# Optimization experiments

Hardware: AMD Instinct MI355X
Metric: run time of the kernel (lower is better)

Reference implementation:

```python
import jax, jax.numpy as jnp
import numpy as np

D = 1024
HEADS = 16
LN_EPS = 1e-5   # torch LayerNorm default
SHEP_EPS = 1e-4 # eps in shepards_MHA
SHEP_P = 2


def setup_inputs() -> dict:
    key = jax.random.key(0)
    k1, k2, k3 = jax.random.split(key, 3)
    b, t, d = 2, 2048, D
    X = jax.random.normal(k1, (b, t, d), dtype=jnp.float32)
    # Linear weights, scaled like torch default init (~U(-1/sqrt(fan_in), ...)) magnitude
    W_in = jax.random.normal(k2, (4 * d, d), dtype=jnp.float32) * (1.0 / np.sqrt(d))
    b_in = jnp.zeros((4 * d,), dtype=jnp.float32)
    W_out = jax.random.normal(k3, (d, d), dtype=jnp.float32) * (1.0 / np.sqrt(d))
    b_out = jnp.zeros((d,), dtype=jnp.float32)
    return {"X": X, "W_in": W_in, "b_in": b_in, "W_out": W_out, "b_out": b_out}


def _shepards_mha(Q, K, V):
    # Q,K,V: [b,h,t,dh]. Euclidean cdist via ||q||^2 + ||k||^2 - 2 q.k
    q2 = jnp.sum(Q * Q, axis=-1, keepdims=True)          # [b,h,t,1]
    k2 = jnp.sum(K * K, axis=-1, keepdims=True)          # [b,h,t,1]
    sq = q2 + jnp.swapaxes(k2, -1, -2) - 2.0 * jnp.einsum('bhqd,bhkd->bhqk', Q, K)
    dist = jnp.sqrt(jnp.maximum(sq, 0.0))                # [b,h,t,t]
    W = (SHEP_EPS + dist) ** (-SHEP_P)
    W = W / (SHEP_EPS + jnp.sum(W, axis=-1, keepdims=True))
    return jnp.einsum('bhqk,bhkd->bhqd', W, V)


def reference(X, W_in, b_in, W_out, b_out):
    b, t, d = X.shape
    h = HEADS
    dh = d // h
    # LayerNorm (no affine)
    mu = jnp.mean(X, axis=-1, keepdims=True)
    var = jnp.mean((X - mu) ** 2, axis=-1, keepdims=True)
    Xn = (X - mu) / jnp.sqrt(var + LN_EPS)
    # project_in: [b,t,4d]
    P = jnp.einsum('btd,ed->bte', Xn, W_in) + b_in
    # [b,t,h,4*dh] -> [b,h,t,4*dh]
    P = P.reshape(b, t, h, 4 * dh).transpose(0, 2, 1, 3)
    Q, K, V, G = jnp.split(P, 4, axis=-1)                # each [b,h,t,dh]
    A = _shepards_mha(Q, K, V)
    O = (G * A).transpose(0, 2, 1, 3).reshape(b, t, d)
    return X + jnp.einsum('btd,ed->bte', O, W_out) + b_out
```

## Files before the change

kernel.cpp:

```cpp
#include <hip/hip_runtime.h>

#define SEQ 2048
#define D_MODEL 1024
#define NTOK 4096
#define PROW 4096
#define DH 64
#define LN_EPS 1e-5f
#define SHEP_EPS 1e-4f

typedef __attribute__((ext_vector_type(8))) short bf16x8;
typedef __attribute__((ext_vector_type(4))) short s16x4;
typedef __attribute__((ext_vector_type(4))) float f32x4;

__device__ __forceinline__ unsigned short f2bf(float f) {
  union { float f; unsigned u; } v; v.f = f;
  unsigned r = v.u + 0x7fffu + ((v.u >> 16) & 1u);
  return (unsigned short)(r >> 16);
}
__device__ __forceinline__ float bf2f(unsigned short s) {
  union { unsigned u; float f; } v; v.u = ((unsigned)s) << 16;
  return v.f;
}
__device__ __forceinline__ void gload16(const void* g, void* l) {
  __builtin_amdgcn_global_load_lds(
      (const __attribute__((address_space(1))) unsigned int*)g,
      (__attribute__((address_space(3))) unsigned int*)l, 16, 0, 0);
}
__device__ __forceinline__ void gload4(const void* g, void* l) {
  __builtin_amdgcn_global_load_lds(
      (const __attribute__((address_space(1))) unsigned int*)g,
      (__attribute__((address_space(3))) unsigned int*)l, 4, 0, 0);
}
__device__ __forceinline__ unsigned cvt_pk_bf16(float lo, float hi) {
  unsigned r;
  asm("v_cvt_pk_bf16_f32 %0, %1, %2" : "=v"(r) : "v"(lo), "v"(hi));
  return r;
}
#define MFMA16(a, b, c) __builtin_amdgcn_mfma_f32_16x16x32_bf16(a, b, c, 0, 0, 0)

__device__ __forceinline__ int xcd_swizzle(int linear, int nwg) {
  int cpx = nwg >> 3;
  return (linear & 7) * cpx + (linear >> 3);
}

__global__ __launch_bounds__(256) void ln_kernel(const float* __restrict__ X,
                                                 unsigned short* __restrict__ Xn) {
  int row = blockIdx.x, tid = threadIdx.x;
  const float4* xr = (const float4*)(X + (size_t)row * D_MODEL);
  float4 v = xr[tid];
  float s = v.x + v.y + v.z + v.w;
  float s2 = v.x * v.x + v.y * v.y + v.z * v.z + v.w * v.w;
#pragma unroll
  for (int off = 32; off > 0; off >>= 1) {
    s += __shfl_down(s, off);
    s2 += __shfl_down(s2, off);
  }
  __shared__ float red[8];
  __shared__ float mb[2];
  int wv = tid >> 6;
  if ((tid & 63) == 0) { red[wv] = s; red[4 + wv] = s2; }
  __syncthreads();
  if (tid == 0) {
    float ts = red[0] + red[1] + red[2] + red[3];
    float t2 = red[4] + red[5] + red[6] + red[7];
    float mu = ts * (1.f / D_MODEL);
    float var = t2 * (1.f / D_MODEL) - mu * mu;
    mb[0] = mu;
    mb[1] = rsqrtf(var + LN_EPS);
  }
  __syncthreads();
  float mu = mb[0], rs = mb[1];
  s16x4 o;
  o[0] = (short)f2bf((v.x - mu) * rs);
  o[1] = (short)f2bf((v.y - mu) * rs);
  o[2] = (short)f2bf((v.z - mu) * rs);
  o[3] = (short)f2bf((v.w - mu) * rs);
  ((s16x4*)(Xn + (size_t)row * D_MODEL))[tid] = o;
}

__global__ __launch_bounds__(256) void cvt_both_kernel(const float* __restrict__ Win,
                                                       const float* __restrict__ Wout,
                                                       unsigned short* __restrict__ dst) {
  const int N1 = (4096 * 1024) / 4;
  const int N2 = (1024 * 1024) / 4;
  int i = blockIdx.x * 256 + threadIdx.x;
  if (i >= N1 + N2) return;
  float4 v = (i < N1) ? ((const float4*)Win)[i] : ((const float4*)Wout)[i - N1];
  s16x4 o;
  o[0] = (short)f2bf(v.x);
  o[1] = (short)f2bf(v.y);
  o[2] = (short)f2bf(v.z);
  o[3] = (short)f2bf(v.w);
  ((s16x4*)dst)[i] = o;
}

__global__ __launch_bounds__(256) void gemm_p_kernel(
    const unsigned short* __restrict__ A, const unsigned short* __restrict__ B,
    const float* __restrict__ bias, unsigned short* __restrict__ C,
    int M, int N, int K) {
  __shared__ __align__(16) unsigned short sA[128 * 32];
  __shared__ __align__(16) unsigned short sB[128 * 32];
  int tid = threadIdx.x;
  int nwg = gridDim.x * gridDim.y;
  int swz = xcd_swizzle(blockIdx.y * gridDim.x + blockIdx.x, nwg);
  int m0 = (swz / gridDim.x) * 128, n0 = (swz % gridDim.x) * 128;
  int wv = tid >> 6, lane = tid & 63;
  int wr = wv >> 1, wc = wv & 1;
  int lr = lane & 15, lq = lane >> 4;
  f32x4 acc[4][4] = {};
  int srow = tid >> 2, scol = (tid & 3) * 8;
  const unsigned short* gA = A + (size_t)(m0 + srow) * K + scol;
  const unsigned short* gB = B + (size_t)(n0 + srow) * K + scol;
  unsigned short* lA = sA + tid * 8;
  unsigned short* lB = sB + tid * 8;
  for (int k0 = 0; k0 < K; k0 += 32) {
    gload16(gA + k0, lA);
    gload16(gA + k0 + (size_t)64 * K, lA + 64 * 32);
    gload16(gB + k0, lB);
    gload16(gB + k0 + (size_t)64 * K, lB + 64 * 32);
    __syncthreads();
    bf16x8 af[4], bfr[4];
#pragma unroll
    for (int m = 0; m < 4; m++)
      af[m] = *(const bf16x8*)&sA[(wr * 64 + m * 16 + lr) * 32 + lq * 8];
#pragma unroll
    for (int n = 0; n < 4; n++)
      bfr[n] = *(const bf16x8*)&sB[(wc * 64 + n * 16 + lr) * 32 + lq * 8];
#pragma unroll
    for (int m = 0; m < 4; m++)
#pragma unroll
      for (int n = 0; n < 4; n++)
        acc[m][n] = MFMA16(af[m], bfr[n], acc[m][n]);
    __syncthreads();
  }
#pragma unroll
  for (int m = 0; m < 4; m++) {
    int row = m0 + wr * 64 + m * 16 + lq * 4;
#pragma unroll
    for (int n = 0; n < 4; n++) {
      int col = n0 + wc * 64 + n * 16 + lr;
      float bv = bias[col];
#pragma unroll
      for (int r = 0; r < 4; r++)
        C[(size_t)(row + r) * N + col] = f2bf(acc[m][n][r] + bv);
    }
  }
}

__global__ __launch_bounds__(256) void gemm_out_kernel(
    const unsigned short* __restrict__ A, const unsigned short* __restrict__ B,
    const float* __restrict__ bias, const float* __restrict__ Xres,
    float* __restrict__ Out, int M, int N, int K) {
  __shared__ __align__(16) unsigned short sA[128 * 32];
  __shared__ __align__(16) unsigned short sB[128 * 32];
  int tid = threadIdx.x;
  int nwg = gridDim.x * gridDim.y;
  int swz = xcd_swizzle(blockIdx.y * gridDim.x + blockIdx.x, nwg);
  int m0 = (swz / gridDim.x) * 128, n0 = (swz % gridDim.x) * 128;
  int wv = tid >> 6, lane = tid & 63;
  int wr = wv >> 1, wc = wv & 1;
  int lr = lane & 15, lq = lane >> 4;
  f32x4 acc[4][4] = {};
  int srow = tid >> 2, scol = (tid & 3) * 8;
  const unsigned short* gA = A + (size_t)(m0 + srow) * K + scol;
  const unsigned short* gB = B + (size_t)(n0 + srow) * K + scol;
  unsigned short* lA = sA + tid * 8;
  unsigned short* lB = sB + tid * 8;
  for (int k0 = 0; k0 < K; k0 += 32) {
    gload16(gA + k0, lA);
    gload16(gA + k0 + (size_t)64 * K, lA + 64 * 32);
    gload16(gB + k0, lB);
    gload16(gB + k0 + (size_t)64 * K, lB + 64 * 32);
    __syncthreads();
    bf16x8 af[4], bfr[4];
#pragma unroll
    for (int m = 0; m < 4; m++)
      af[m] = *(const bf16x8*)&sA[(wr * 64 + m * 16 + lr) * 32 + lq * 8];
#pragma unroll
    for (int n = 0; n < 4; n++)
      bfr[n] = *(const bf16x8*)&sB[(wc * 64 + n * 16 + lr) * 32 + lq * 8];
#pragma unroll
    for (int m = 0; m < 4; m++)
#pragma unroll
      for (int n = 0; n < 4; n++)
        acc[m][n] = MFMA16(af[m], bfr[n], acc[m][n]);
    __syncthreads();
  }
#pragma unroll
  for (int m = 0; m < 4; m++) {
    int row = m0 + wr * 64 + m * 16 + lq * 4;
#pragma unroll
    for (int n = 0; n < 4; n++) {
      int col = n0 + wc * 64 + n * 16 + lr;
      float bv = bias[col];
#pragma unroll
      for (int r = 0; r < 4; r++) {
        size_t idx = (size_t)(row + r) * N + col;
        Out[idx] = Xres[idx] + acc[m][n][r] + bv;
      }
    }
  }
}

__global__ __launch_bounds__(256) void transv_kernel(const unsigned short* __restrict__ P,
                                                     unsigned short* __restrict__ Vt) {
  int kt = blockIdx.x;
  int bh = blockIdx.y;
  int b = bh >> 4, h = bh & 15;
  __shared__ unsigned short sT[64][72];
  int tid = threadIdx.x;
  const unsigned short* vbase = P + ((size_t)(b * SEQ + kt * 64)) * PROW + h * 256 + 128;
#pragma unroll
  for (int it = 0; it < 2; it++) {
    int c = tid + it * 256;
    int k = c >> 3, c0 = (c & 7) * 8;
    uint4 u = *(const uint4*)(vbase + (size_t)k * PROW + c0);
    unsigned e[4] = {u.x, u.y, u.z, u.w};
#pragma unroll
    for (int j = 0; j < 4; j++) {
      sT[c0 + 2 * j][k] = (unsigned short)(e[j] & 0xffffu);
      sT[c0 + 2 * j + 1][k] = (unsigned short)(e[j] >> 16);
    }
  }
  __syncthreads();
  unsigned short* obase = Vt + (size_t)bh * 64 * SEQ + kt * 64;
#pragma unroll
  for (int it = 0; it < 2; it++) {
    int cc = tid + it * 256;
    int crow = cc >> 3, k0 = (cc & 7) * 8;
    uint4 o;
    unsigned short e[8];
#pragma unroll
    for (int j = 0; j < 8; j++) e[j] = sT[crow][k0 + j];
    o.x = (unsigned)e[0] | ((unsigned)e[1] << 16);
    o.y = (unsigned)e[2] | ((unsigned)e[3] << 16);
    o.z = (unsigned)e[4] | ((unsigned)e[5] << 16);
    o.w = (unsigned)e[6] | ((unsigned)e[7] << 16);
    *(uint4*)(obase + (size_t)crow * SEQ + k0) = o;
  }
}

__global__ __launch_bounds__(256) void norms_kernel(const unsigned short* __restrict__ P,
                                                    float* __restrict__ nrm) {
  int id = blockIdx.x * 256 + threadIdx.x;
  int bh = id >> 12;
  int which = (id >> 11) & 1;
  int t = id & 2047;
  int b = bh >> 4, h = bh & 15;
  const unsigned short* p = P + ((size_t)(b * SEQ + t)) * PROW + h * 256 + which * 64;
  const uint4* pv = (const uint4*)p;
  float acc = 0.f;
#pragma unroll
  for (int i = 0; i < 8; i++) {
    uint4 u = pv[i];
    unsigned arr[4] = {u.x, u.y, u.z, u.w};
#pragma unroll
    for (int j = 0; j < 4; j++) {
      float lo = __uint_as_float(arr[j] << 16);
      float hi = __uint_as_float(arr[j] & 0xffff0000u);
      acc += lo * lo + hi * hi;
    }
  }
  nrm[(size_t)(bh * 2 + which) * SEQ + t] = acc;
}

__global__ __launch_bounds__(512) void attn_kernel(
    const unsigned short* __restrict__ P, const unsigned short* __restrict__ Vt,
    const float* __restrict__ nrm, unsigned short* __restrict__ O) {
  int qt = blockIdx.x, bh = blockIdx.y;
  int b = bh >> 4, h = bh & 15;
  int tid = threadIdx.x;
  int w = tid >> 6, lane = tid & 63;
  int lr = lane & 15, lq = lane >> 4;

  __shared__ __align__(16) unsigned short sQ[128 * 64];
  __shared__ __align__(16) unsigned short sK[2][64 * 64];
  __shared__ __align__(16) unsigned short sV[2][64 * 64];
  __shared__ __align__(16) unsigned short sW[128 * 64];
  __shared__ __align__(16) float sK2[2][64];
  __shared__ __align__(16) float sDen[8][16];

  const unsigned short* qbase = P + ((size_t)(b * SEQ + qt * 128)) * PROW + h * 256;
  const unsigned short* kbase = P + ((size_t)(b * SEQ)) * PROW + h * 256 + 64;
  const unsigned short* vtb = Vt + (size_t)bh * 64 * SEQ;
  const float* k2base = nrm + (size_t)(bh * 2 + 1) * SEQ;

  int srow = tid >> 3;
  int scol = ((tid & 7) ^ (srow & 7)) * 8;
  const unsigned short* kSrc = kbase + (size_t)srow * PROW + scol;
  const unsigned short* vSrc = vtb + (size_t)srow * SEQ + scol;

#pragma unroll
  for (int it = 0; it < 2; it++) {
    int c = tid + it * 512;
    int row = c >> 3;
    int col = ((c & 7) ^ (row & 7)) * 8;
    gload16(qbase + (size_t)row * PROW + col, (char*)sQ + c * 16);
  }
  gload16(kSrc, (char*)&sK[0][0] + tid * 16);
  gload16(vSrc, (char*)&sV[0][0] + tid * 16);
  if (w == 0) gload4(k2base + lane, (char*)&sK2[0][0] + lane * 4);
  float q2 = nrm[(size_t)(bh * 2) * SEQ + qt * 128 + 16 * w + lr];
  __syncthreads();

  int qrow = 16 * w + lr;
  bf16x8 qf[2];
#pragma unroll
  for (int ks = 0; ks < 2; ks++)
    qf[ks] = *(const bf16x8*)((const char*)sQ + qrow * 128 +
                              ((ks * 64 + lq * 16) ^ ((lr & 7) << 4)));

  f32x4 num[4] = {};
  float den = 0.f;
  char* wrow = (char*)sW + qrow * 128;

  for (int kt = 0; kt < SEQ / 64; kt++) {
    int cur = kt & 1, nxt = cur ^ 1;
    if (kt < SEQ / 64 - 1) {
      gload16(kSrc + (size_t)(kt + 1) * 64 * PROW, (char*)&sK[nxt][0] + tid * 16);
      gload16(vSrc + (size_t)(kt + 1) * 64, (char*)&sV[nxt][0] + tid * 16);
      if (w == 0) gload4(k2base + (kt + 1) * 64 + lane, (char*)&sK2[nxt][0] + lane * 4);
    }

    f32x4 st[4] = {};
    __builtin_amdgcn_s_setprio(1);
#pragma unroll
    for (int fk = 0; fk < 4; fk++) {
      int row = 16 * fk + lr;
      const char* krow = (const char*)&sK[cur][0] + row * 128;
      bf16x8 kf0 = *(const bf16x8*)(krow + ((lq * 16) ^ ((row & 7) << 4)));
      bf16x8 kf1 = *(const bf16x8*)(krow + ((64 + lq * 16) ^ ((row & 7) << 4)));
      st[fk] = MFMA16(kf0, qf[0], st[fk]);
      st[fk] = MFMA16(kf1, qf[1], st[fk]);
    }
    __builtin_amdgcn_s_setprio(0);

#pragma unroll
    for (int fk = 0; fk < 4; fk++) {
      f32x4 k2v = *(const f32x4*)&sK2[cur][16 * fk + 4 * lq];
      float w0 = __builtin_amdgcn_rcpf(fmaxf(fmaf(-2.f, st[fk][0], q2 + k2v[0]), 1e-8f));
      float w1 = __builtin_amdgcn_rcpf(fmaxf(fmaf(-2.f, st[fk][1], q2 + k2v[1]), 1e-8f));
      float w2 = __builtin_amdgcn_rcpf(fmaxf(fmaf(-2.f, st[fk][2], q2 + k2v[2]), 1e-8f));
      float w3 = __builtin_amdgcn_rcpf(fmaxf(fmaf(-2.f, st[fk][3], q2 + k2v[3]), 1e-8f));
      den += (w0 + w1) + (w2 + w3);
      uint2 pp;
      pp.x = cvt_pk_bf16(w0, w1);
      pp.y = cvt_pk_bf16(w2, w3);
      *(uint2*)(wrow + ((32 * fk + 8 * lq) ^ ((lr & 7) << 4))) = pp;
    }

    __builtin_amdgcn_s_setprio(1);
#pragma unroll
    for (int ks = 0; ks < 2; ks++) {
      bf16x8 aw = *(const bf16x8*)(wrow + ((64 * ks + 16 * lq) ^ ((lr & 7) << 4)));
#pragma unroll
      for (int fn = 0; fn < 4; fn++) {
        int row = 16 * fn + lr;
        bf16x8 bv = *(const bf16x8*)((const char*)&sV[cur][0] + row * 128 +
                                     ((64 * ks + 16 * lq) ^ ((row & 7) << 4)));
        num[fn] = MFMA16(aw, bv, num[fn]);
      }
    }
    __builtin_amdgcn_s_setprio(0);
    __syncthreads();
  }

  den += __shfl_xor(den, 16);
  den += __shfl_xor(den, 32);
  if (lq == 0) sDen[w][lr] = den;
  __syncthreads();
  f32x4 dv = *(const f32x4*)&sDen[w][4 * lq];
  f32x4 rdv;
#pragma unroll
  for (int r = 0; r < 4; r++) rdv[r] = __builtin_amdgcn_rcpf(dv[r] + SHEP_EPS);

  const unsigned short* gbase = qbase + 192;
#pragma unroll
  for (int fn = 0; fn < 4; fn++) {
    int c = 16 * fn + lr;
#pragma unroll
    for (int r = 0; r < 4; r++) {
      int ql = 16 * w + 4 * lq + r;
      float g = bf2f(gbase[(size_t)ql * PROW + c]);
      float a = num[fn][r] * rdv[r];
      O[((size_t)(b * SEQ + qt * 128 + ql)) * D_MODEL + h * DH + c] = f2bf(g * a);
    }
  }
}

extern "C" void kernel_launch(void* const* d_in, const int* in_sizes, int n_in,
                              void* d_out, int out_size, void* d_ws, size_t ws_size,
                              hipStream_t stream) {
  const float* X = (const float*)d_in[0];
  const float* W_in = (const float*)d_in[1];
  const float* b_in = (const float*)d_in[2];
  const float* W_out = (const float*)d_in[3];
  const float* b_out = (const float*)d_in[4];
  float* out = (float*)d_out;

  char* ws = (char*)d_ws;
  unsigned short* Xn = (unsigned short*)(ws);
  unsigned short* O = (unsigned short*)(ws);
  unsigned short* Wi = (unsigned short*)(ws + ((size_t)8 << 20));
  unsigned short* Vt = (unsigned short*)(ws + ((size_t)8 << 20));
  unsigned short* Wo = (unsigned short*)(ws + ((size_t)16 << 20));
  unsigned short* P = (unsigned short*)(ws + ((size_t)18 << 20));
  float* nrm = (float*)(ws + ((size_t)50 << 20));

  ln_kernel<<<NTOK, 256, 0, stream>>>(X, Xn);
  cvt_both_kernel<<<5120, 256, 0, stream>>>(W_in, W_out, Wi);
  gemm_p_kernel<<<dim3(32, 32), 256, 0, stream>>>(Xn, Wi, b_in, P, 4096, 4096, 1024);
  transv_kernel<<<dim3(32, 32), 256, 0, stream>>>(P, Vt);
  norms_kernel<<<512, 256, 0, stream>>>(P, nrm);
  attn_kernel<<<dim3(16, 32), 512, 0, stream>>>(P, Vt, nrm, O);
  gemm_out_kernel<<<dim3(8, 32), 256, 0, stream>>>(O, Wo, b_out, X, out, 4096, 1024, 1024);
}
```

Before: 170.3 us.

## Double GEMM K-tile to 64 with XOR-swizzled LDS layout

```diff
diff --git a/kernel.cpp b/kernel.cpp
--- a/kernel.cpp
+++ b/kernel.cpp
@@ -98,8 +98,8 @@
     const unsigned short* __restrict__ A, const unsigned short* __restrict__ B,
     const float* __restrict__ bias, unsigned short* __restrict__ C,
     int M, int N, int K) {
-  __shared__ __align__(16) unsigned short sA[128 * 32];
-  __shared__ __align__(16) unsigned short sB[128 * 32];
+  __shared__ __align__(16) unsigned short sA[128 * 64];
+  __shared__ __align__(16) unsigned short sB[128 * 64];
   int tid = threadIdx.x;
   int nwg = gridDim.x * gridDim.y;
   int swz = xcd_swizzle(blockIdx.y * gridDim.x + blockIdx.x, nwg);
@@ -108,29 +108,37 @@
   int wr = wv >> 1, wc = wv & 1;
   int lr = lane & 15, lq = lane >> 4;
   f32x4 acc[4][4] = {};
-  int srow = tid >> 2, scol = (tid & 3) * 8;
-  const unsigned short* gA = A + (size_t)(m0 + srow) * K + scol;
-  const unsigned short* gB = B + (size_t)(n0 + srow) * K + scol;
-  unsigned short* lA = sA + tid * 8;
-  unsigned short* lB = sB + tid * 8;
-  for (int k0 = 0; k0 < K; k0 += 32) {
-    gload16(gA + k0, lA);
-    gload16(gA + k0 + (size_t)64 * K, lA + 64 * 32);
-    gload16(gB + k0, lB);
-    gload16(gB + k0 + (size_t)64 * K, lB + 64 * 32);
+  for (int k0 = 0; k0 < K; k0 += 64) {
+#pragma unroll
+    for (int it = 0; it < 4; it++) {
+      int c = tid + it * 256;
+      int row = c >> 3;
+      int col = ((c & 7) ^ (row & 7)) * 8;
+      gload16(A + (size_t)(m0 + row) * K + k0 + col, (char*)sA + c * 16);
+      gload16(B + (size_t)(n0 + row) * K + k0 + col, (char*)sB + c * 16);
+    }
     __syncthreads();
-    bf16x8 af[4], bfr[4];
-#pragma unroll
-    for (int m = 0; m < 4; m++)
-      af[m] = *(const bf16x8*)&sA[(wr * 64 + m * 16 + lr) * 32 + lq * 8];
-#pragma unroll
-    for (int n = 0; n < 4; n++)
-      bfr[n] = *(const bf16x8*)&sB[(wc * 64 + n * 16 + lr) * 32 + lq * 8];
-#pragma unroll
-    for (int m = 0; m < 4; m++)
-#pragma unroll
-      for (int n = 0; n < 4; n++)
-        acc[m][n] = MFMA16(af[m], bfr[n], acc[m][n]);
+#pragma unroll
+    for (int ks = 0; ks < 2; ks++) {
+      bf16x8 af[4], bfr[4];
+#pragma unroll
+      for (int m = 0; m < 4; m++) {
+        int row = wr * 64 + m * 16 + lr;
+        af[m] = *(const bf16x8*)((const char*)sA + row * 128 +
+                                 (((ks * 4 + lq) ^ (lr & 7)) * 16));
+      }
+#pragma unroll
+      for (int n = 0; n < 4; n++) {
+        int row = wc * 64 + n * 16 + lr;
+        bfr[n] = *(const bf16x8*)((const char*)sB + row * 128 +
+                                  (((ks * 4 + lq) ^ (lr & 7)) * 16));
+      }
+#pragma unroll
+      for (int m = 0; m < 4; m++)
+#pragma unroll
+        for (int n = 0; n < 4; n++)
+          acc[m][n] = MFMA16(af[m], bfr[n], acc[m][n]);
+    }
     __syncthreads();
   }
 #pragma unroll
@@ -151,8 +159,8 @@
     const unsigned short* __restrict__ A, const unsigned short* __restrict__ B,
     const float* __restrict__ bias, const float* __restrict__ Xres,
     float* __restrict__ Out, int M, int N, int K) {
-  __shared__ __align__(16) unsigned short sA[128 * 32];
-  __shared__ __align__(16) unsigned short sB[128 * 32];
+  __shared__ __align__(16) unsigned short sA[128 * 64];
+  __shared__ __align__(16) unsigned short sB[128 * 64];
   int tid = threadIdx.x;
   int nwg = gridDim.x * gridDim.y;
   int swz = xcd_swizzle(blockIdx.y * gridDim.x + blockIdx.x, nwg);
@@ -161,29 +169,37 @@
   int wr = wv >> 1, wc = wv & 1;
   int lr = lane & 15, lq = lane >> 4;
   f32x4 acc[4][4] = {};
-  int srow = tid >> 2, scol = (tid & 3) * 8;
-  const unsigned short* gA = A + (size_t)(m0 + srow) * K + scol;
-  const unsigned short* gB = B + (size_t)(n0 + srow) * K + scol;
-  unsigned short* lA = sA + tid * 8;
-  unsigned short* lB = sB + tid * 8;
-  for (int k0 = 0; k0 < K; k0 += 32) {
-    gload16(gA + k0, lA);
-    gload16(gA + k0 + (size_t)64 * K, lA + 64 * 32);
-    gload16(gB + k0, lB);
-    gload16(gB + k0 + (size_t)64 * K, lB + 64 * 32);
+  for (int k0 = 0; k0 < K; k0 += 64) {
+#pragma unroll
+    for (int it = 0; it < 4; it++) {
+      int c = tid + it * 256;
+      int row = c >> 3;
+      int col = ((c & 7) ^ (row & 7)) * 8;
+      gload16(A + (size_t)(m0 + row) * K + k0 + col, (char*)sA + c * 16);
+      gload16(B + (size_t)(n0 + row) * K + k0 + col, (char*)sB + c * 16);
+    }
     __syncthreads();
-    bf16x8 af[4], bfr[4];
-#pragma unroll
-    for (int m = 0; m < 4; m++)
-      af[m] = *(const bf16x8*)&sA[(wr * 64 + m * 16 + lr) * 32 + lq * 8];
-#pragma unroll
-    for (int n = 0; n < 4; n++)
-      bfr[n] = *(const bf16x8*)&sB[(wc * 64 + n * 16 + lr) * 32 + lq * 8];
-#pragma unroll
-    for (int m = 0; m < 4; m++)
-#pragma unroll
-      for (int n = 0; n < 4; n++)
-        acc[m][n] = MFMA16(af[m], bfr[n], acc[m][n]);
+#pragma unroll
+    for (int ks = 0; ks < 2; ks++) {
+      bf16x8 af[4], bfr[4];
+#pragma unroll
+      for (int m = 0; m < 4; m++) {
+        int row = wr * 64 + m * 16 + lr;
+        af[m] = *(const bf16x8*)((const char*)sA + row * 128 +
+                                 (((ks * 4 + lq) ^ (lr & 7)) * 16));
+      }
+#pragma unroll
+      for (int n = 0; n < 4; n++) {
+        int row = wc * 64 + n * 16 + lr;
+        bfr[n] = *(const bf16x8*)((const char*)sB + row * 128 +
+                                  (((ks * 4 + lq) ^ (lr & 7)) * 16));
+      }
+#pragma unroll
+      for (int m = 0; m < 4; m++)
+#pragma unroll
+        for (int n = 0; n < 4; n++)
+          acc[m][n] = MFMA16(af[m], bfr[n], acc[m][n]);
+    }
     __syncthreads();
   }
 #pragma unroll
```

New measurement: 154.7 us. 1.1x faster.
